# Performance work log

Measured on AMD Instinct MI355X. Metric: run time of the kernel, lower is better.

## Reference

```python
import jax, jax.numpy as jnp
import numpy as np

N_NODES = 50000
N_HEDGES = 10000
NNZ = 640000
D_IN, D_HID, D_OUT = 128, 128, 128


def _glorot(key, fan_in, fan_out):
    s = jnp.sqrt(6.0 / (fan_in + fan_out)).astype(jnp.float32)
    return jax.random.uniform(key, (fan_in, fan_out), jnp.float32, -s, s)


def setup_inputs() -> dict:
    key = jax.random.key(0)
    k_x, k_r, k_c, k_w1, k_w2 = jax.random.split(key, 5)
    x = jax.random.normal(k_x, (N_NODES, D_IN), jnp.float32)
    row = jax.random.randint(k_r, (NNZ,), 0, N_NODES)  # node indices
    col = jax.random.randint(k_c, (NNZ,), 0, N_HEDGES)  # hyperedge indices
    edge_index = jnp.stack([row, col]).astype(jnp.int64)
    return {
        "x": x,
        "edge_index": edge_index,
        "W1": _glorot(k_w1, D_IN, D_HID),
        "b1": jnp.zeros((D_HID,), jnp.float32),
        "W2": _glorot(k_w2, D_HID, D_OUT),
        "b2": jnp.zeros((D_OUT,), jnp.float32),
    }


def _hconv(x, W, b, row, col):
    # PyG HypergraphConv (no attention): out = D^{-1} H B^{-1} H^T (X W) + b
    xw = x @ W  # [N, F_out]
    ones = jnp.ones(row.shape[0], xw.dtype)
    deg_n = jax.ops.segment_sum(ones, row, num_segments=N_NODES)    # node degree D
    deg_e = jax.ops.segment_sum(ones, col, num_segments=N_HEDGES)   # hyperedge degree B
    d_inv = jnp.where(deg_n > 0, 1.0 / deg_n, 0.0)
    b_inv = jnp.where(deg_e > 0, 1.0 / deg_e, 0.0)
    # node -> hyperedge aggregation: m_e = B^{-1} sum_{i in e} (XW)_i
    m = jax.ops.segment_sum(xw[row], col, num_segments=N_HEDGES) * b_inv[:, None]
    # hyperedge -> node aggregation: out_i = D^{-1} sum_{e ni i} m_e
    out = jax.ops.segment_sum(m[col], row, num_segments=N_NODES) * d_inv[:, None]
    return out + b


def reference(x, edge_index, W1, b1, W2, b2):
    row, col = edge_index[0], edge_index[1]
    h = jax.nn.relu(_hconv(x, W1, b1, row, col))  # dropout inactive in eval
    return _hconv(h, W2, b2, row, col)
```

## Files before the change

### kernel.cpp

```cpp
#include <hip/hip_runtime.h>
#include <hip/hip_bf16.h>

#define D 128
#define N_HEDGES 10000
#define PART_CHUNKS 128
#define CAP_N 64
#define CAP_E 192
#define CSTRIDE 16

__global__ __launch_bounds__(256) void build_part(const int* __restrict__ row,
                                                  const int* __restrict__ col,
                                                  int* __restrict__ cnt_n,
                                                  int* __restrict__ cnt_e,
                                                  ushort* __restrict__ pad_n,
                                                  ushort* __restrict__ pad_e,
                                                  int nnz, int N, int E) {
    int xcd = blockIdx.x & 7;
    int chunk = blockIdx.x >> 3;
    int csz = (nnz + PART_CHUNKS - 1) / PART_CHUNKS;
    int lo = chunk * csz;
    int hi = min(lo + csz, nnz);
    int nlo = (int)((long)N * xcd >> 3), nhi = (int)((long)N * (xcd + 1) >> 3);
    int elo = (int)((long)E * xcd >> 3), ehi = (int)((long)E * (xcd + 1) >> 3);
    for (int i = lo + threadIdx.x; i < hi; i += 256) {
        int r = row[i], c = col[i];
        if (r >= nlo && r < nhi) {
            int pn = atomicAdd(&cnt_n[(size_t)r * CSTRIDE], 1);
            if (pn < CAP_N) pad_n[(size_t)r * CAP_N + pn] = (ushort)c;
        }
        if (c >= elo && c < ehi) {
            int pe = atomicAdd(&cnt_e[(size_t)c * CSTRIDE], 1);
            if (pe < CAP_E) pad_e[(size_t)c * CAP_E + pe] = (ushort)r;
        }
    }
}

__global__ __launch_bounds__(256, 2) void gemm128(const float* __restrict__ X,
                                                  const float* __restrict__ W,
                                                  float* __restrict__ Y, int M) {
    __shared__ float Wl[D * D];
    __shared__ float Xl[32 * D];
    int t = threadIdx.x;
    int block_row = blockIdx.x * 32;

    const float4* W4 = (const float4*)W;
    float4* Wl4 = (float4*)Wl;
#pragma unroll
    for (int i = 0; i < 16; ++i) Wl4[t + 256 * i] = W4[t + 256 * i];

    int rows = M - block_row; if (rows > 32) rows = 32;
#pragma unroll
    for (int i = 0; i < 4; ++i) {
        int idx = t + 256 * i;
        int r = idx >> 5, c4 = idx & 31;
        float4 v = make_float4(0.f, 0.f, 0.f, 0.f);
        if (r < rows) v = ((const float4*)(X + (size_t)(block_row + r) * D))[c4];
        ((float4*)Xl)[idx] = v;
    }
    __syncthreads();

    int cp = t & 63;
    int rg = t >> 6;
    float2 acc[8];
#pragma unroll
    for (int r = 0; r < 8; ++r) acc[r] = make_float2(0.f, 0.f);

    const float* xbase = Xl + (rg * 8) * D;
#pragma unroll 2
    for (int k4 = 0; k4 < 32; ++k4) {
        float2 wv0 = ((const float2*)(Wl + (k4 * 4 + 0) * D))[cp];
        float2 wv1 = ((const float2*)(Wl + (k4 * 4 + 1) * D))[cp];
        float2 wv2 = ((const float2*)(Wl + (k4 * 4 + 2) * D))[cp];
        float2 wv3 = ((const float2*)(Wl + (k4 * 4 + 3) * D))[cp];
#pragma unroll
        for (int r = 0; r < 8; ++r) {
            float4 xv = ((const float4*)(xbase + r * D))[k4];
            acc[r].x += xv.x * wv0.x; acc[r].y += xv.x * wv0.y;
            acc[r].x += xv.y * wv1.x; acc[r].y += xv.y * wv1.y;
            acc[r].x += xv.z * wv2.x; acc[r].y += xv.z * wv2.y;
            acc[r].x += xv.w * wv3.x; acc[r].y += xv.w * wv3.y;
        }
    }
#pragma unroll
    for (int r = 0; r < 8; ++r) {
        int row = block_row + rg * 8 + r;
        if (row < M) ((float2*)(Y + (size_t)row * D))[cp] = acc[r];
    }
}

__global__ __launch_bounds__(256) void edge_agg(const float* __restrict__ src,
                                                const ushort* __restrict__ pad,
                                                const int* __restrict__ cnt,
                                                float* __restrict__ dst, int nseg) {
    int w = (blockIdx.x * 256 + threadIdx.x) >> 6;
    int lane = threadIdx.x & 63;
    if (w >= nseg) return;
    int len = min(cnt[(size_t)w * CSTRIDE], CAP_E);
    const ushort* list = pad + (size_t)w * CAP_E;
    int half = lane >> 5;
    int c4 = lane & 31;
    float4 a0 = make_float4(0.f, 0.f, 0.f, 0.f);
    float4 a1 = make_float4(0.f, 0.f, 0.f, 0.f);
    int i = 0;
#pragma unroll 2
    for (; i + 4 <= len; i += 4) {
        int r0 = list[i + half];
        int r1 = list[i + 2 + half];
        float4 v0 = ((const float4*)(src + (size_t)r0 * D))[c4];
        float4 v1 = ((const float4*)(src + (size_t)r1 * D))[c4];
        a0.x += v0.x; a0.y += v0.y; a0.z += v0.z; a0.w += v0.w;
        a1.x += v1.x; a1.y += v1.y; a1.z += v1.z; a1.w += v1.w;
    }
    if (i + 2 <= len) {
        int r = list[i + half];
        float4 v = ((const float4*)(src + (size_t)r * D))[c4];
        a0.x += v.x; a0.y += v.y; a0.z += v.z; a0.w += v.w;
        i += 2;
    }
    if (i < len && half == 0) {
        int r = list[i];
        float4 v = ((const float4*)(src + (size_t)r * D))[c4];
        a1.x += v.x; a1.y += v.y; a1.z += v.z; a1.w += v.w;
    }
    a0.x += a1.x; a0.y += a1.y; a0.z += a1.z; a0.w += a1.w;
    a0.x += __shfl_xor(a0.x, 32);
    a0.y += __shfl_xor(a0.y, 32);
    a0.z += __shfl_xor(a0.z, 32);
    a0.w += __shfl_xor(a0.w, 32);
    if (half == 0) {
        float sc = (len > 0) ? (1.0f / (float)len) : 0.0f;
        ((float4*)(dst + (size_t)w * D))[c4] =
            make_float4(a0.x * sc, a0.y * sc, a0.z * sc, a0.w * sc);
    }
}

template <bool RELU>
__global__ __launch_bounds__(256) void node_agg(const float* __restrict__ src,
                                                const ushort* __restrict__ pad,
                                                const int* __restrict__ cnt,
                                                const float* __restrict__ bias,
                                                float* __restrict__ dst, int nseg) {
    int w = (blockIdx.x * 256 + threadIdx.x) >> 6;
    int lane = threadIdx.x & 63;
    if (w >= nseg) return;
    int len = min(cnt[(size_t)w * CSTRIDE], CAP_N);
    const ushort* list = pad + (size_t)w * CAP_N;
    int half = lane >> 5;
    int c4 = lane & 31;
    float4 a0 = make_float4(0.f, 0.f, 0.f, 0.f);
    float4 a1 = make_float4(0.f, 0.f, 0.f, 0.f);
    int i = 0;
#pragma unroll 2
    for (; i + 4 <= len; i += 4) {
        int r0 = list[i + half];
        int r1 = list[i + 2 + half];
        float4 v0 = ((const float4*)(src + (size_t)r0 * D))[c4];
        float4 v1 = ((const float4*)(src + (size_t)r1 * D))[c4];
        a0.x += v0.x; a0.y += v0.y; a0.z += v0.z; a0.w += v0.w;
        a1.x += v1.x; a1.y += v1.y; a1.z += v1.z; a1.w += v1.w;
    }
    if (i + 2 <= len) {
        int r = list[i + half];
        float4 v = ((const float4*)(src + (size_t)r * D))[c4];
        a0.x += v.x; a0.y += v.y; a0.z += v.z; a0.w += v.w;
        i += 2;
    }
    if (i < len && half == 0) {
        int r = list[i];
        float4 v = ((const float4*)(src + (size_t)r * D))[c4];
        a1.x += v.x; a1.y += v.y; a1.z += v.z; a1.w += v.w;
    }
    a0.x += a1.x; a0.y += a1.y; a0.z += a1.z; a0.w += a1.w;
    a0.x += __shfl_xor(a0.x, 32);
    a0.y += __shfl_xor(a0.y, 32);
    a0.z += __shfl_xor(a0.z, 32);
    a0.w += __shfl_xor(a0.w, 32);
    if (half == 0) {
        float sc = (len > 0) ? (1.0f / (float)len) : 0.0f;
        float4 bv = ((const float4*)bias)[c4];
        float ox = a0.x * sc + bv.x;
        float oy = a0.y * sc + bv.y;
        float oz = a0.z * sc + bv.z;
        float ow = a0.w * sc + bv.w;
        if (RELU) {
            ox = fmaxf(ox, 0.f); oy = fmaxf(oy, 0.f);
            oz = fmaxf(oz, 0.f); ow = fmaxf(ow, 0.f);
        }
        ((float4*)(dst + (size_t)w * D))[c4] = make_float4(ox, oy, oz, ow);
    }
}

extern "C" void kernel_launch(void* const* d_in, const int* in_sizes, int n_in,
                              void* d_out, int out_size, void* d_ws, size_t ws_size,
                              hipStream_t stream) {
    const float* x  = (const float*)d_in[0];
    const int*   ei = (const int*)d_in[1];
    const float* W1 = (const float*)d_in[2];
    const float* b1 = (const float*)d_in[3];
    const float* W2 = (const float*)d_in[4];
    const float* b2 = (const float*)d_in[5];
    float* out = (float*)d_out;

    const int NNZ = in_sizes[1] / 2;
    const int N   = in_sizes[0] / D;
    const int E   = N_HEDGES;

    const int* row = ei;
    const int* col = ei + NNZ;

    char* p = (char*)d_ws;
    auto alloc = [&](size_t bytes) {
        char* r = p;
        p += (bytes + 255) & ~(size_t)255;
        return r;
    };
    float*  s     = (float*)alloc(sizeof(float) * (size_t)E * D);
    float*  m     = (float*)alloc(sizeof(float) * (size_t)E * D);
    ushort* pad_n = (ushort*)alloc(sizeof(ushort) * (size_t)N * CAP_N);
    ushort* pad_e = (ushort*)alloc(sizeof(ushort) * (size_t)E * CAP_E);
    char*   zstart = p;
    int*    cnt_n = (int*)alloc(sizeof(int) * (size_t)N * CSTRIDE);
    int*    cnt_e = (int*)alloc(sizeof(int) * (size_t)E * CSTRIDE);
    size_t  zbytes = (size_t)(p - zstart);

    hipMemsetAsync(zstart, 0, zbytes, stream);

    build_part<<<8 * PART_CHUNKS, 256, 0, stream>>>(row, col, cnt_n, cnt_e,
                                                    pad_n, pad_e, NNZ, N, E);

    int gemm_blocks = (E + 31) / 32;
    int eblk = (E + 3) / 4;
    int nblk = (N + 3) / 4;

    edge_agg<<<eblk, 256, 0, stream>>>(x, pad_e, cnt_e, s, E);
    gemm128<<<gemm_blocks, 256, 0, stream>>>(s, W1, m, E);
    node_agg<true><<<nblk, 256, 0, stream>>>(m, pad_n, cnt_n, b1, out, N);

    edge_agg<<<eblk, 256, 0, stream>>>(out, pad_e, cnt_e, s, E);
    gemm128<<<gemm_blocks, 256, 0, stream>>>(s, W2, m, E);
    node_agg<false><<<nblk, 256, 0, stream>>>(m, pad_n, cnt_n, b2, out, N);
}
```

Baseline: 306.9 us.

## Store gathered intermediates in bf16 to halve gather traffic

Converts x to bf16 in a new pre-pass and makes the GEMM outputs and the hidden layer bf16, so all four gather-aggregation kernels read half the bytes per row. Accumulation stays in fp32 and the final output stays fp32. This adds a conversion kernel over x and extra rounding error in the intermediates, and it reuses the output buffer as bf16 scratch for the hidden layer.

```diff
diff --git a/kernel.cpp b/kernel.cpp
--- a/kernel.cpp
+++ b/kernel.cpp
@@ -7,6 +7,26 @@
 #define CAP_N 64
 #define CAP_E 192
 #define CSTRIDE 16
+
+__device__ __forceinline__ float bf2f(ushort u) {
+    union { unsigned int i; float f; } v; v.i = ((unsigned int)u) << 16; return v.f;
+}
+__device__ __forceinline__ ushort f2bf(float f) {
+    union { float f; unsigned int i; } v; v.f = f;
+    unsigned int r = v.i + 0x7FFFu + ((v.i >> 16) & 1u);
+    return (ushort)(r >> 16);
+}
+
+__global__ __launch_bounds__(256) void f32_to_bf16(const float* __restrict__ in,
+                                                   ushort* __restrict__ out, int n4) {
+    int i = blockIdx.x * 256 + threadIdx.x;
+    if (i < n4) {
+        float4 v = ((const float4*)in)[i];
+        ushort4 o;
+        o.x = f2bf(v.x); o.y = f2bf(v.y); o.z = f2bf(v.z); o.w = f2bf(v.w);
+        ((ushort4*)out)[i] = o;
+    }
+}
 
 __global__ __launch_bounds__(256) void build_part(const int* __restrict__ row,
                                                   const int* __restrict__ col,
@@ -35,9 +55,9 @@
     }
 }
 
-__global__ __launch_bounds__(256, 2) void gemm128(const float* __restrict__ X,
-                                                  const float* __restrict__ W,
-                                                  float* __restrict__ Y, int M) {
+__global__ __launch_bounds__(256, 2) void gemm128_bf(const float* __restrict__ X,
+                                                     const float* __restrict__ W,
+                                                     ushort* __restrict__ Y, int M) {
     __shared__ float Wl[D * D];
     __shared__ float Xl[32 * D];
     int t = threadIdx.x;
@@ -84,11 +104,14 @@
 #pragma unroll
     for (int r = 0; r < 8; ++r) {
         int row = block_row + rg * 8 + r;
-        if (row < M) ((float2*)(Y + (size_t)row * D))[cp] = acc[r];
-    }
-}
-
-__global__ __launch_bounds__(256) void edge_agg(const float* __restrict__ src,
+        if (row < M) {
+            ushort2 o; o.x = f2bf(acc[r].x); o.y = f2bf(acc[r].y);
+            ((ushort2*)(Y + (size_t)row * D))[cp] = o;
+        }
+    }
+}
+
+__global__ __launch_bounds__(256) void edge_agg(const ushort* __restrict__ src,
                                                 const ushort* __restrict__ pad,
                                                 const int* __restrict__ cnt,
                                                 float* __restrict__ dst, int nseg) {
@@ -106,21 +129,21 @@
     for (; i + 4 <= len; i += 4) {
         int r0 = list[i + half];
         int r1 = list[i + 2 + half];
-        float4 v0 = ((const float4*)(src + (size_t)r0 * D))[c4];
-        float4 v1 = ((const float4*)(src + (size_t)r1 * D))[c4];
-        a0.x += v0.x; a0.y += v0.y; a0.z += v0.z; a0.w += v0.w;
-        a1.x += v1.x; a1.y += v1.y; a1.z += v1.z; a1.w += v1.w;
+        ushort4 u0 = ((const ushort4*)(src + (size_t)r0 * D))[c4];
+        ushort4 u1 = ((const ushort4*)(src + (size_t)r1 * D))[c4];
+        a0.x += bf2f(u0.x); a0.y += bf2f(u0.y); a0.z += bf2f(u0.z); a0.w += bf2f(u0.w);
+        a1.x += bf2f(u1.x); a1.y += bf2f(u1.y); a1.z += bf2f(u1.z); a1.w += bf2f(u1.w);
     }
     if (i + 2 <= len) {
         int r = list[i + half];
-        float4 v = ((const float4*)(src + (size_t)r * D))[c4];
-        a0.x += v.x; a0.y += v.y; a0.z += v.z; a0.w += v.w;
+        ushort4 u = ((const ushort4*)(src + (size_t)r * D))[c4];
+        a0.x += bf2f(u.x); a0.y += bf2f(u.y); a0.z += bf2f(u.z); a0.w += bf2f(u.w);
         i += 2;
     }
     if (i < len && half == 0) {
         int r = list[i];
-        float4 v = ((const float4*)(src + (size_t)r * D))[c4];
-        a1.x += v.x; a1.y += v.y; a1.z += v.z; a1.w += v.w;
+        ushort4 u = ((const ushort4*)(src + (size_t)r * D))[c4];
+        a1.x += bf2f(u.x); a1.y += bf2f(u.y); a1.z += bf2f(u.z); a1.w += bf2f(u.w);
     }
     a0.x += a1.x; a0.y += a1.y; a0.z += a1.z; a0.w += a1.w;
     a0.x += __shfl_xor(a0.x, 32);
@@ -135,11 +158,11 @@
 }
 
 template <bool RELU>
-__global__ __launch_bounds__(256) void node_agg(const float* __restrict__ src,
+__global__ __launch_bounds__(256) void node_agg(const ushort* __restrict__ src,
                                                 const ushort* __restrict__ pad,
                                                 const int* __restrict__ cnt,
                                                 const float* __restrict__ bias,
-                                                float* __restrict__ dst, int nseg) {
+                                                void* __restrict__ dst, int nseg) {
     int w = (blockIdx.x * 256 + threadIdx.x) >> 6;
     int lane = threadIdx.x & 63;
     if (w >= nseg) return;
@@ -154,21 +177,21 @@
     for (; i + 4 <= len; i += 4) {
         int r0 = list[i + half];
         int r1 = list[i + 2 + half];
-        float4 v0 = ((const float4*)(src + (size_t)r0 * D))[c4];
-        float4 v1 = ((const float4*)(src + (size_t)r1 * D))[c4];
-        a0.x += v0.x; a0.y += v0.y; a0.z += v0.z; a0.w += v0.w;
-        a1.x += v1.x; a1.y += v1.y; a1.z += v1.z; a1.w += v1.w;
+        ushort4 u0 = ((const ushort4*)(src + (size_t)r0 * D))[c4];
+        ushort4 u1 = ((const ushort4*)(src + (size_t)r1 * D))[c4];
+        a0.x += bf2f(u0.x); a0.y += bf2f(u0.y); a0.z += bf2f(u0.z); a0.w += bf2f(u0.w);
+        a1.x += bf2f(u1.x); a1.y += bf2f(u1.y); a1.z += bf2f(u1.z); a1.w += bf2f(u1.w);
     }
     if (i + 2 <= len) {
         int r = list[i + half];
-        float4 v = ((const float4*)(src + (size_t)r * D))[c4];
-        a0.x += v.x; a0.y += v.y; a0.z += v.z; a0.w += v.w;
+        ushort4 u = ((const ushort4*)(src + (size_t)r * D))[c4];
+        a0.x += bf2f(u.x); a0.y += bf2f(u.y); a0.z += bf2f(u.z); a0.w += bf2f(u.w);
         i += 2;
     }
     if (i < len && half == 0) {
         int r = list[i];
-        float4 v = ((const float4*)(src + (size_t)r * D))[c4];
-        a1.x += v.x; a1.y += v.y; a1.z += v.z; a1.w += v.w;
+        ushort4 u = ((const ushort4*)(src + (size_t)r * D))[c4];
+        a1.x += bf2f(u.x); a1.y += bf2f(u.y); a1.z += bf2f(u.z); a1.w += bf2f(u.w);
     }
     a0.x += a1.x; a0.y += a1.y; a0.z += a1.z; a0.w += a1.w;
     a0.x += __shfl_xor(a0.x, 32);
@@ -185,8 +208,12 @@
         if (RELU) {
             ox = fmaxf(ox, 0.f); oy = fmaxf(oy, 0.f);
             oz = fmaxf(oz, 0.f); ow = fmaxf(ow, 0.f);
-        }
-        ((float4*)(dst + (size_t)w * D))[c4] = make_float4(ox, oy, oz, ow);
+            ushort4 o;
+            o.x = f2bf(ox); o.y = f2bf(oy); o.z = f2bf(oz); o.w = f2bf(ow);
+            ((ushort4*)((ushort*)dst + (size_t)w * D))[c4] = o;
+        } else {
+            ((float4*)((float*)dst + (size_t)w * D))[c4] = make_float4(ox, oy, oz, ow);
+        }
     }
 }
 
@@ -215,28 +242,31 @@
         return r;
     };
     float*  s     = (float*)alloc(sizeof(float) * (size_t)E * D);
-    float*  m     = (float*)alloc(sizeof(float) * (size_t)E * D);
+    ushort* m_bf  = (ushort*)alloc(sizeof(ushort) * (size_t)E * D);
+    ushort* xh    = (ushort*)alloc(sizeof(ushort) * (size_t)N * D);
     ushort* pad_n = (ushort*)alloc(sizeof(ushort) * (size_t)N * CAP_N);
     ushort* pad_e = (ushort*)alloc(sizeof(ushort) * (size_t)E * CAP_E);
     char*   zstart = p;
     int*    cnt_n = (int*)alloc(sizeof(int) * (size_t)N * CSTRIDE);
     int*    cnt_e = (int*)alloc(sizeof(int) * (size_t)E * CSTRIDE);
     size_t  zbytes = (size_t)(p - zstart);
+    ushort* hh = (ushort*)d_out;
 
     hipMemsetAsync(zstart, 0, zbytes, stream);
 
     build_part<<<8 * PART_CHUNKS, 256, 0, stream>>>(row, col, cnt_n, cnt_e,
                                                     pad_n, pad_e, NNZ, N, E);
+    f32_to_bf16<<<(N * D / 4 + 255) / 256, 256, 0, stream>>>(x, xh, N * D / 4);
 
     int gemm_blocks = (E + 31) / 32;
     int eblk = (E + 3) / 4;
     int nblk = (N + 3) / 4;
 
-    edge_agg<<<eblk, 256, 0, stream>>>(x, pad_e, cnt_e, s, E);
-    gemm128<<<gemm_blocks, 256, 0, stream>>>(s, W1, m, E);
-    node_agg<true><<<nblk, 256, 0, stream>>>(m, pad_n, cnt_n, b1, out, N);
-
-    edge_agg<<<eblk, 256, 0, stream>>>(out, pad_e, cnt_e, s, E);
-    gemm128<<<gemm_blocks, 256, 0, stream>>>(s, W2, m, E);
-    node_agg<false><<<nblk, 256, 0, stream>>>(m, pad_n, cnt_n, b2, out, N);
-}
+    edge_agg<<<eblk, 256, 0, stream>>>(xh, pad_e, cnt_e, s, E);
+    gemm128_bf<<<gemm_blocks, 256, 0, stream>>>(s, W1, m_bf, E);
+    node_agg<true><<<nblk, 256, 0, stream>>>(m_bf, pad_n, cnt_n, b1, hh, N);
+
+    edge_agg<<<eblk, 256, 0, stream>>>(hh, pad_e, cnt_e, s, E);
+    gemm128_bf<<<gemm_blocks, 256, 0, stream>>>(s, W2, m_bf, E);
+    node_agg<false><<<nblk, 256, 0, stream>>>(m_bf, pad_n, cnt_n, b2, out, N);
+}
```

New measurement: 262.3 us. 14.5% less time.
